# Optimization experiments

Measured on AMD Instinct MI355X. Metric: run time of the kernel, lower is better.

The kernel has to match this reference:

```python
import jax, jax.numpy as jnp
import numpy as np

B, L, T, IN, H, OUT = 1024, 64, 128, 13, 64, 13
NEG = -1e30


def gru_step(x, h, Wih, Whh, bih, bhh):
    # PyTorch GRU cell: gates ordered (r, z, n)
    gi = x @ Wih.T + bih          # [B, 3H]
    gh = h @ Whh.T + bhh          # [B, 3H]
    ir, iz, inn = jnp.split(gi, 3, axis=-1)
    hr, hz, hn = jnp.split(gh, 3, axis=-1)
    r = jax.nn.sigmoid(ir + hr)
    z = jax.nn.sigmoid(iz + hz)
    n = jnp.tanh(inn + r * hn)
    return (1.0 - z) * n + z * h


def setup_inputs() -> dict:
    key = jax.random.key(0)
    ks = jax.random.split(key, 10)
    s = float(1.0 / np.sqrt(H))
    x = jax.random.normal(ks[0], (B, L, IN), jnp.float32)
    lengths = jax.random.randint(ks[1], (B,), 1, L + 1).at[0].set(L)
    Wih = jax.random.uniform(ks[2], (3 * H, IN), jnp.float32, -s, s)
    Whh = jax.random.uniform(ks[3], (3 * H, H), jnp.float32, -s, s)
    bih = jax.random.uniform(ks[4], (3 * H,), jnp.float32, -s, s)
    bhh = jax.random.uniform(ks[5], (3 * H,), jnp.float32, -s, s)
    Wf = jax.random.uniform(ks[6], (OUT, H), jnp.float32, -s, s)
    bf = jax.random.uniform(ks[7], (OUT,), jnp.float32, -s, s)
    Wa = jax.random.uniform(ks[8], (H, H), jnp.float32, -s, s)
    ba = jax.random.uniform(ks[9], (H,), jnp.float32, -s, s)
    return dict(x=x, lengths=lengths, output_length=T, Wih=Wih, Whh=Whh,
                bih=bih, bhh=bhh, Wf=Wf, bf=bf, Wa=Wa, ba=ba)


def reference(x, lengths, output_length, Wih, Whh, bih, bhh, Wf, bf, Wa, ba):
    b, l = x.shape[0], x.shape[1]
    xT = jnp.swapaxes(x, 0, 1)                        # [L, B, IN]
    h0 = jnp.zeros((b, H), x.dtype)

    # Encoder: masked GRU emulating pack_padded/pad_packed semantics:
    # hidden frozen past each sequence's length; outputs zero past length.
    def enc(h, inp):
        t, xt = inp
        hn = gru_step(xt, h, Wih, Whh, bih, bhh)
        valid = (t < lengths)[:, None]
        h = jnp.where(valid, hn, h)
        return h, jnp.where(valid, hn, 0.0)

    h, outs = jax.lax.scan(enc, h0, (jnp.arange(l), xT))
    # output[:, -1, :] of the padded output (zeros for seqs shorter than max)
    nin = outs[-1] @ Wf.T + bf                        # [B, OUT]

    Tn = output_length
    buf0 = jnp.zeros((Tn, b, H), x.dtype)             # growing past-prediction buffer

    def dec(carry, t):
        h, buf, nin = carry
        hn = gru_step(nin, h, Wih, Whh, bih, bhh)     # output_lstm == hidden (1 layer, 1 step)
        # attention recomputed over all past predictions (softmax over time axis)
        logits = jnp.einsum('tbh,gh->tbg', buf, Wa) + ba      # [T, B, H]
        logits = jnp.where((jnp.arange(Tn) < t)[:, None, None], logits, NEG)
        w = jax.nn.softmax(logits, axis=0)
        o = hn + jnp.sum(w * buf, axis=0)             # at t=0 buffer is all zeros -> +0
        y = o @ Wf.T + bf
        return (hn, buf.at[t].set(o), y), y

    _, ys = jax.lax.scan(dec, (h, buf0, nin), jnp.arange(Tn))
    return jnp.swapaxes(ys, 0, 1)                     # [B, T, OUT]
```

## Files before the change

kernel.cpp:

```cpp
#include <hip/hip_runtime.h>
#include <stdint.h>
#include <math.h>

#define BATCH 1024
#define SEQL  64
#define TDEC  128
#define NIN   13
#define NH    64
#define NOUT  13

typedef _Float16 h2 __attribute__((ext_vector_type(2)));
typedef __fp16   g2 __attribute__((ext_vector_type(2)));

union FU  { uint32_t u; float f; };
union HU  { uint16_t u; _Float16 h; };
union H2U { uint32_t u; h2 h; g2 g; };

__device__ __forceinline__ float bf2f(uint16_t v) { FU t; t.u = ((uint32_t)v) << 16; return t.f; }
__device__ __forceinline__ float hf2f(uint16_t v) { HU t; t.u = v; return (float)t.h; }

__device__ __forceinline__ float ldf(const void* p, long i, int mode) {
    if (mode == 1) return bf2f(((const uint16_t*)p)[i]);
    if (mode == 2) return hf2f(((const uint16_t*)p)[i]);
    return ((const float*)p)[i];
}

__device__ __forceinline__ bool pass_stats(const void* p, int n, int lane, int mode,
                                           float band_lo, float band_hi, float max_ok) {
    int m = (n + 1) / 2;
    int cnt = (m < 64) ? m : 64;
    bool ok_max = true, in_band = false;
    if (lane < cnt) {
        long pos = 2L * (((long)lane * m) / cnt);
        float v = (mode == 1) ? bf2f(((const uint16_t*)p)[pos])
                              : hf2f(((const uint16_t*)p)[pos]);
        float a = fabsf(v);
        ok_max  = (a <= max_ok);
        in_band = (a >= band_lo && a <= band_hi);
    }
    bool allmax = __all(ok_max);
    int nb = (int)__popcll(__ballot(in_band));
    int need = cnt / 4; if (need < 1) need = 1;
    return allmax && (nb >= need);
}
__device__ __forceinline__ int detect(const void* p, int n, int lane,
                                      float band_lo, float band_hi, float max_ok) {
    if (pass_stats(p, n, lane, 1, band_lo, band_hi, max_ok)) return 1;
    if (pass_stats(p, n, lane, 2, band_lo, band_hi, max_ok)) return 2;
    return 0;
}
__device__ __forceinline__ bool detect_len64(const int* p, int lane) {
    int v = p[2 * lane + 1];
    return __all(v == 0);
}

__device__ __forceinline__ float dot2(h2 a, h2 b, float c) {
#if __has_builtin(__builtin_amdgcn_fdot2)
    return __builtin_amdgcn_fdot2(a, b, c, false);
#else
    return c + (float)a[0] * (float)b[0] + (float)a[1] * (float)b[1];
#endif
}
__device__ __forceinline__ uint32_t pku(float a, float b) {
    H2U t; t.g = __builtin_amdgcn_cvt_pkrtz(a, b); return t.u;
}
__device__ __forceinline__ h2 uh(uint32_t u) { H2U t; t.u = u; return t.h; }
__device__ __forceinline__ float rcp_(float x) { return __builtin_amdgcn_rcpf(x); }
__device__ __forceinline__ float sigm(float x)  { return rcp_(1.0f + __expf(-x)); }
__device__ __forceinline__ float tanh_(float x) { return 1.0f - 2.0f * rcp_(__expf(2.0f * x) + 1.0f); }
__device__ __forceinline__ void wb() { __builtin_amdgcn_wave_barrier(); }

#define BCAST32(vreg, dst)                                                 \
    {                                                                      \
        float _vx = __shfl_xor((vreg), 1);                                 \
        uint32_t _pr = pku((vreg), _vx);                                   \
        _Pragma("unroll")                                                  \
        for (int _k = 0; _k < 32; ++_k)                                    \
            (dst)[_k] = __builtin_amdgcn_readlane(_pr, 2 * _k);            \
    }

__global__ __launch_bounds__(64, 1)
void gru_attn_kernel(const void* __restrict__ x, const int* __restrict__ lengths,
                     const void* __restrict__ Wih, const void* __restrict__ Whh,
                     const void* __restrict__ bih, const void* __restrict__ bhh,
                     const void* __restrict__ Wf, const void* __restrict__ bfv,
                     const void* __restrict__ Wa, const void* __restrict__ ba,
                     float* __restrict__ out)
{
    const int b = blockIdx.x;
    const int j = threadIdx.x;

    __shared__ __align__(16) uint32_t xs2[SEQL][8];

    const int dX   = detect(x,   BATCH * SEQL * NIN, j, 0.25f, 4.0f, 16.0f);
    const int dWih = detect(Wih, 3 * NH * NIN, j, 0.04f, 0.13f, 0.14f);
    const int dWhh = detect(Whh, 3 * NH * NH,  j, 0.04f, 0.13f, 0.14f);
    const int dBih = detect(bih, 3 * NH,       j, 0.04f, 0.13f, 0.14f);
    const int dBhh = detect(bhh, 3 * NH,       j, 0.04f, 0.13f, 0.14f);
    const int dWf  = detect(Wf,  NOUT * NH,    j, 0.04f, 0.13f, 0.14f);
    const int dBf  = detect(bfv, NOUT,         j, 0.04f, 0.13f, 0.14f);
    const int dWa  = detect(Wa,  NH * NH,      j, 0.04f, 0.13f, 0.14f);
    const int dBa  = detect(ba,  NH,           j, 0.04f, 0.13f, 0.14f);
    const bool len64 = detect_len64(lengths, j);

    h2 wihr[7], wihz[7], wihn[7];
    h2 whhr[32], whhz[32], whhn[32];
    h2 wap[32], wfp[32];

#pragma unroll
    for (int k = 0; k < 7; ++k) {
        float a0 = ldf(Wih, (0 * NH + j) * NIN + 2 * k, dWih);
        float a1 = (2 * k + 1 < NIN) ? ldf(Wih, (0 * NH + j) * NIN + 2 * k + 1, dWih) : 0.0f;
        wihr[k] = uh(pku(a0, a1));
        float b0 = ldf(Wih, (1 * NH + j) * NIN + 2 * k, dWih);
        float b1 = (2 * k + 1 < NIN) ? ldf(Wih, (1 * NH + j) * NIN + 2 * k + 1, dWih) : 0.0f;
        wihz[k] = uh(pku(b0, b1));
        float c0 = ldf(Wih, (2 * NH + j) * NIN + 2 * k, dWih);
        float c1 = (2 * k + 1 < NIN) ? ldf(Wih, (2 * NH + j) * NIN + 2 * k + 1, dWih) : 0.0f;
        wihn[k] = uh(pku(c0, c1));
    }
    const int jf = (j < NOUT) ? j : 0;
#pragma unroll
    for (int k = 0; k < 32; ++k) {
        whhr[k] = uh(pku(ldf(Whh, (0 * NH + j) * NH + 2 * k, dWhh),
                         ldf(Whh, (0 * NH + j) * NH + 2 * k + 1, dWhh)));
        whhz[k] = uh(pku(ldf(Whh, (1 * NH + j) * NH + 2 * k, dWhh),
                         ldf(Whh, (1 * NH + j) * NH + 2 * k + 1, dWhh)));
        whhn[k] = uh(pku(ldf(Whh, (2 * NH + j) * NH + 2 * k, dWhh),
                         ldf(Whh, (2 * NH + j) * NH + 2 * k + 1, dWhh)));
        wap[k]  = uh(pku(ldf(Wa, j * NH + 2 * k, dWa),
                         ldf(Wa, j * NH + 2 * k + 1, dWa)));
        wfp[k]  = uh(pku(ldf(Wf, jf * NH + 2 * k, dWf),
                         ldf(Wf, jf * NH + 2 * k + 1, dWf)));
    }

    const float bcr = ldf(bih, j, dBih)          + ldf(bhh, j, dBhh);
    const float bcz = ldf(bih, NH + j, dBih)     + ldf(bhh, NH + j, dBhh);
    const float bni = ldf(bih, 2 * NH + j, dBih);
    const float bnh = ldf(bhh, 2 * NH + j, dBhh);
    const float baj = ldf(ba, j, dBa);
    const float bfj = ldf(bfv, jf, dBf);
    const int len = len64 ? lengths[2 * b] : lengths[b];

    {
        const long base = ((long)b * SEQL + j) * NIN;
        float v[14];
#pragma unroll
        for (int k = 0; k < NIN; ++k) v[k] = ldf(x, base + k, dX);
        v[13] = 0.0f;
#pragma unroll
        for (int p = 0; p < 7; ++p) xs2[j][p] = pku(v[2 * p], v[2 * p + 1]);
        xs2[j][7] = 0u;
    }
    wb();

    float h = 0.0f;
    float out_last = 0.0f;

    uint32_t hpk[32];
    BCAST32(h, hpk);

#pragma unroll 1
    for (int t = 0; t < SEQL; ++t) {
        uint4 q0 = *(const uint4*)xs2[t];
        uint4 q1 = *(const uint4*)(xs2[t] + 4);

        float ar = bcr, az = bcz, an = bni, hna = bnh;
        float arb = 0.0f, azb = 0.0f, hnb = 0.0f;
#pragma unroll
        for (int k = 0; k < 32; ++k) {
            h2 hv = uh(hpk[k]);
            if (k & 1) { arb = dot2(whhr[k], hv, arb); azb = dot2(whhz[k], hv, azb); hnb = dot2(whhn[k], hv, hnb); }
            else       { ar  = dot2(whhr[k], hv, ar);  az  = dot2(whhz[k], hv, az);  hna = dot2(whhn[k], hv, hna); }
        }
        {
            uint32_t xw[8] = {q0.x, q0.y, q0.z, q0.w, q1.x, q1.y, q1.z, q1.w};
#pragma unroll
            for (int p = 0; p < 7; ++p) {
                h2 xv = uh(xw[p]);
                ar = dot2(wihr[p], xv, ar);
                az = dot2(wihz[p], xv, az);
                an = dot2(wihn[p], xv, an);
            }
        }
        ar += arb; az += azb; hna += hnb;
        float r = sigm(ar);
        float z = sigm(az);
        float n = tanh_(an + r * hna);
        float hnew = n + z * (h - n);
        if (t < len) h = hnew;
        if (t == SEQL - 1) out_last = (t < len) ? hnew : 0.0f;
        BCAST32(h, hpk);
    }

    uint32_t ypk[7];
    {
        uint32_t opk[32];
        BCAST32(out_last, opk);
        float nv = bfj, nv2 = 0.0f;
#pragma unroll
        for (int k = 0; k < 32; ++k) {
            h2 ov = uh(opk[k]);
            if (k & 1) nv2 = dot2(wfp[k], ov, nv2);
            else       nv  = dot2(wfp[k], ov, nv);
        }
        nv += nv2;
        float nz = (j < NOUT) ? nv : 0.0f;
        float np = __shfl_xor(nz, 1);
        uint32_t pr = pku(nz, np);
#pragma unroll
        for (int k = 0; k < 7; ++k) ypk[k] = __builtin_amdgcn_readlane(pr, 2 * k);
    }

    float m = -1e30f, Zs = 0.0f, num = 0.0f;

#pragma unroll 1
    for (int t = 0; t < TDEC; ++t) {
        float ar = bcr, az = bcz, an = bni, hna = bnh;
        float arb = 0.0f, azb = 0.0f, hnb = 0.0f;
#pragma unroll
        for (int k = 0; k < 32; ++k) {
            h2 hv = uh(hpk[k]);
            if (k & 1) { arb = dot2(whhr[k], hv, arb); azb = dot2(whhz[k], hv, azb); hnb = dot2(whhn[k], hv, hnb); }
            else       { ar  = dot2(whhr[k], hv, ar);  az  = dot2(whhz[k], hv, az);  hna = dot2(whhn[k], hv, hna); }
        }
#pragma unroll
        for (int p = 0; p < 7; ++p) {
            h2 xv = uh(ypk[p]);
            ar = dot2(wihr[p], xv, ar);
            az = dot2(wihz[p], xv, az);
            an = dot2(wihn[p], xv, an);
        }
        ar += arb; az += azb; hna += hnb;
        float r = sigm(ar);
        float z = sigm(az);
        float n = tanh_(an + r * hna);
        float hnew = n + z * (h - n);
        h = hnew;
        float attn = (t > 0) ? num * rcp_(Zs) : 0.0f;
        float o = hnew + attn;

        BCAST32(hnew, hpk);
        uint32_t opk[32];
        BCAST32(o, opk);

        float s = baj, yv = bfj, s2 = 0.0f, y2 = 0.0f;
#pragma unroll
        for (int k = 0; k < 32; ++k) {
            h2 ov = uh(opk[k]);
            if (k & 1) { s2 = dot2(wap[k], ov, s2); y2 = dot2(wfp[k], ov, y2); }
            else       { s  = dot2(wap[k], ov, s);  yv = dot2(wfp[k], ov, yv); }
        }
        s += s2; yv += y2;
        float mn = fmaxf(m, s);
        float al = __expf(m - mn);
        float p  = __expf(s - mn);
        Zs  = Zs * al + p;
        num = num * al + p * o;
        m = mn;
        if (j < NOUT) out[((size_t)b * TDEC + t) * NOUT + j] = yv;
        float yz = (j < NOUT) ? yv : 0.0f;
        float yp = __shfl_xor(yz, 1);
        uint32_t pr = pku(yz, yp);
#pragma unroll
        for (int k = 0; k < 7; ++k) ypk[k] = __builtin_amdgcn_readlane(pr, 2 * k);
    }
}

extern "C" void kernel_launch(void* const* d_in, const int* in_sizes, int n_in,
                              void* d_out, int out_size, void* d_ws, size_t ws_size,
                              hipStream_t stream) {
    (void)in_sizes; (void)n_in; (void)out_size; (void)d_ws; (void)ws_size;
    const void* x      = d_in[0];
    const int* lengths = (const int*)d_in[1];
    const void* Wih = d_in[3];
    const void* Whh = d_in[4];
    const void* bih = d_in[5];
    const void* bhh = d_in[6];
    const void* Wf  = d_in[7];
    const void* bf  = d_in[8];
    const void* Wa  = d_in[9];
    const void* ba  = d_in[10];
    float* out = (float*)d_out;

    gru_attn_kernel<<<dim3(BATCH), dim3(64), 0, stream>>>(
        x, lengths, Wih, Whh, bih, bhh, Wf, bf, Wa, ba, out);
}
```

Before: 226.7 us.

## Fold output projection into decoder input weights and use DPP lane swap

Precomputes Wih·Wf as fused per-lane weights (plus the Wih·bf bias) so the decoder feeds the broadcast o vector straight into the GRU input gates. This removes the per-step y broadcast (shuffle plus readlanes) from the serial dependency chain. The trade-off is 96 extra fp16 weight registers and 96 dot2 per step in place of 21, which raises register pressure and ALU work. The xor-1 shuffle inside the broadcast macro is also replaced with a DPP quad-permute move.

Result: slower. 439.4 us (+93.8%).

```diff
diff --git a/kernel.cpp b/kernel.cpp
--- a/kernel.cpp
+++ b/kernel.cpp
@@ -70,10 +70,15 @@
 __device__ __forceinline__ float tanh_(float x) { return 1.0f - 2.0f * rcp_(__expf(2.0f * x) + 1.0f); }
 __device__ __forceinline__ void wb() { __builtin_amdgcn_wave_barrier(); }
 
+__device__ __forceinline__ float swap1(float v) {
+    FU a; a.f = v;
+    FU b; b.u = (uint32_t)__builtin_amdgcn_mov_dpp((int)a.u, 0xB1, 0xF, 0xF, true);
+    return b.f;
+}
+
 #define BCAST32(vreg, dst)                                                 \
     {                                                                      \
-        float _vx = __shfl_xor((vreg), 1);                                 \
-        uint32_t _pr = pku((vreg), _vx);                                   \
+        uint32_t _pr = pku((vreg), swap1(vreg));                           \
         _Pragma("unroll")                                                  \
         for (int _k = 0; _k < 32; ++_k)                                    \
             (dst)[_k] = __builtin_amdgcn_readlane(_pr, 2 * _k);            \
@@ -106,6 +111,7 @@
     h2 wihr[7], wihz[7], wihn[7];
     h2 whhr[32], whhz[32], whhn[32];
     h2 wap[32], wfp[32];
+    h2 wfur[32], wfuz[32], wfun[32];
 
 #pragma unroll
     for (int k = 0; k < 7; ++k) {
@@ -134,12 +140,40 @@
                          ldf(Wf, jf * NH + 2 * k + 1, dWf)));
     }
 
+    float bxr = 0.0f, bxz = 0.0f, bxn = 0.0f;
+    {
+        float wr[NIN], wz[NIN], wn[NIN];
+#pragma unroll
+        for (int i = 0; i < NIN; ++i) {
+            wr[i] = ldf(Wih, (0 * NH + j) * NIN + i, dWih);
+            wz[i] = ldf(Wih, (1 * NH + j) * NIN + i, dWih);
+            wn[i] = ldf(Wih, (2 * NH + j) * NIN + i, dWih);
+            float bfi = ldf(bfv, i, dBf);
+            bxr += wr[i] * bfi; bxz += wz[i] * bfi; bxn += wn[i] * bfi;
+        }
+        for (int k = 0; k < 32; ++k) {
+            float r0 = 0.0f, r1 = 0.0f, z0 = 0.0f, z1 = 0.0f, n0 = 0.0f, n1 = 0.0f;
+#pragma unroll
+            for (int i = 0; i < NIN; ++i) {
+                float w0 = ldf(Wf, i * NH + 2 * k, dWf);
+                float w1 = ldf(Wf, i * NH + 2 * k + 1, dWf);
+                r0 = fmaf(wr[i], w0, r0); r1 = fmaf(wr[i], w1, r1);
+                z0 = fmaf(wz[i], w0, z0); z1 = fmaf(wz[i], w1, z1);
+                n0 = fmaf(wn[i], w0, n0); n1 = fmaf(wn[i], w1, n1);
+            }
+            wfur[k] = uh(pku(r0, r1));
+            wfuz[k] = uh(pku(z0, z1));
+            wfun[k] = uh(pku(n0, n1));
+        }
+    }
+
     const float bcr = ldf(bih, j, dBih)          + ldf(bhh, j, dBhh);
     const float bcz = ldf(bih, NH + j, dBih)     + ldf(bhh, NH + j, dBhh);
     const float bni = ldf(bih, 2 * NH + j, dBih);
     const float bnh = ldf(bhh, 2 * NH + j, dBhh);
     const float baj = ldf(ba, j, dBa);
     const float bfj = ldf(bfv, jf, dBf);
+    const float bcrD = bcr + bxr, bczD = bcz + bxz, bniD = bni + bxn;
     const int len = len64 ? lengths[2 * b] : lengths[b];
 
     {
@@ -193,31 +227,16 @@
         BCAST32(h, hpk);
     }
 
-    uint32_t ypk[7];
-    {
-        uint32_t opk[32];
-        BCAST32(out_last, opk);
-        float nv = bfj, nv2 = 0.0f;
-#pragma unroll
-        for (int k = 0; k < 32; ++k) {
-            h2 ov = uh(opk[k]);
-            if (k & 1) nv2 = dot2(wfp[k], ov, nv2);
-            else       nv  = dot2(wfp[k], ov, nv);
-        }
-        nv += nv2;
-        float nz = (j < NOUT) ? nv : 0.0f;
-        float np = __shfl_xor(nz, 1);
-        uint32_t pr = pku(nz, np);
-#pragma unroll
-        for (int k = 0; k < 7; ++k) ypk[k] = __builtin_amdgcn_readlane(pr, 2 * k);
-    }
+    uint32_t opk[32];
+    BCAST32(out_last, opk);
 
     float m = -1e30f, Zs = 0.0f, num = 0.0f;
 
 #pragma unroll 1
     for (int t = 0; t < TDEC; ++t) {
-        float ar = bcr, az = bcz, an = bni, hna = bnh;
+        float ar = bcrD, az = bczD, an = bniD, hna = bnh;
         float arb = 0.0f, azb = 0.0f, hnb = 0.0f;
+        float arc = 0.0f, azc = 0.0f, anc = 0.0f;
 #pragma unroll
         for (int k = 0; k < 32; ++k) {
             h2 hv = uh(hpk[k]);
@@ -225,13 +244,12 @@
             else       { ar  = dot2(whhr[k], hv, ar);  az  = dot2(whhz[k], hv, az);  hna = dot2(whhn[k], hv, hna); }
         }
 #pragma unroll
-        for (int p = 0; p < 7; ++p) {
-            h2 xv = uh(ypk[p]);
-            ar = dot2(wihr[p], xv, ar);
-            az = dot2(wihz[p], xv, az);
-            an = dot2(wihn[p], xv, an);
-        }
-        ar += arb; az += azb; hna += hnb;
+        for (int k = 0; k < 32; ++k) {
+            h2 ov = uh(opk[k]);
+            if (k & 1) { arc = dot2(wfur[k], ov, arc); azc = dot2(wfuz[k], ov, azc); anc = dot2(wfun[k], ov, anc); }
+            else       { ar  = dot2(wfur[k], ov, ar);  az  = dot2(wfuz[k], ov, az);  an  = dot2(wfun[k], ov, an); }
+        }
+        ar += arb + arc; az += azb + azc; an += anc; hna += hnb;
         float r = sigm(ar);
         float z = sigm(az);
         float n = tanh_(an + r * hna);
@@ -241,7 +259,6 @@
         float o = hnew + attn;
 
         BCAST32(hnew, hpk);
-        uint32_t opk[32];
         BCAST32(o, opk);
 
         float s = baj, yv = bfj, s2 = 0.0f, y2 = 0.0f;
@@ -259,11 +276,6 @@
         num = num * al + p * o;
         m = mn;
         if (j < NOUT) out[((size_t)b * TDEC + t) * NOUT + j] = yv;
-        float yz = (j < NOUT) ? yv : 0.0f;
-        float yp = __shfl_xor(yz, 1);
-        uint32_t pr = pku(yz, yp);
-#pragma unroll
-        for (int k = 0; k < 7; ++k) ypk[k] = __builtin_amdgcn_readlane(pr, 2 * k);
     }
 }
 
```
